# Performance work log

Measured on AMD Instinct MI355X. Metric: run time of the kernel, lower is better.

The kernel has to match this reference:

```python
import jax, jax.numpy as jnp
import numpy as np

N = 100000        # nodes
E = 3200000       # directed edges (already includes both directions per the repo)
F_IN = 256
HID = 16
C = 40


def setup_inputs() -> dict:
    key = jax.random.key(0)
    k = jax.random.split(key, 5)
    x = jax.random.normal(k[0], (N, F_IN), dtype=jnp.float32)
    edge_index = jax.random.randint(k[1], (2, E), 0, N, dtype=jnp.int64)
    W1 = jax.random.normal(k[2], (F_IN, HID), dtype=jnp.float32) * (1.0 / np.sqrt(F_IN))
    b1 = jnp.zeros((HID,), jnp.float32)
    W2 = jax.random.normal(k[3], (HID, C), dtype=jnp.float32) * (1.0 / np.sqrt(HID))
    b2 = jnp.zeros((C,), jnp.float32)
    return {"x": x, "edge_index": edge_index, "W1": W1, "b1": b1, "W2": W2, "b2": b2}


def reference(x, edge_index, W1, b1, W2, b2):
    n = x.shape[0]
    # GCNConv: add self-loops, symmetric degree normalization (shared by both layers)
    loop = jnp.arange(n, dtype=edge_index.dtype)
    src = jnp.concatenate([edge_index[0], loop])
    dst = jnp.concatenate([edge_index[1], loop])
    deg = jax.ops.segment_sum(jnp.ones_like(dst, x.dtype), dst, num_segments=n)
    dinv = jnp.where(deg > 0, jax.lax.rsqrt(deg), 0.0)
    norm = dinv[src] * dinv[dst]  # [E+N]

    def gcn(h, W, b):
        h = h @ W  # transform first (PyG order), keeps edge messages low-dim
        msg = h[src] * norm[:, None]
        return jax.ops.segment_sum(msg, dst, num_segments=n) + b

    h = jax.nn.relu(gcn(x, W1, b1))
    # dropout is identity in eval mode (training=False)
    logits = gcn(h, W2, b2)
    return jax.nn.log_softmax(logits, axis=1)
```

## Files before the change

### kernel.cpp

```cpp
#include <hip/hip_runtime.h>
#include <hip/hip_bf16.h>


#define BSH 7
#define NPB 128
#define BCAP 4736
#define MAXB 1024
#define OVF_CAP 8192
#define EPB 4096

#define SCALE 2097152.0f
#define INVS  4.76837158203125e-7f

typedef __attribute__((ext_vector_type(8))) short bf16x8;
typedef __attribute__((ext_vector_type(4))) short bf16x4;
typedef __attribute__((ext_vector_type(4))) float f32x4;

__device__ __forceinline__ short f2b(float f) {
    __hip_bfloat16 h = __float2bfloat16(f);
    return *reinterpret_cast<short*>(&h);
}
__device__ __forceinline__ float b2f(short s) {
    return __uint_as_float(((unsigned int)(unsigned short)s) << 16);
}

__global__ __launch_bounds__(512) void binA(
        const int* __restrict__ src, const int* __restrict__ dst,
        int* __restrict__ gcur, int* __restrict__ padded,
        int2* __restrict__ ovf, int* __restrict__ ovf_cnt, int E) {
    __shared__ int hist[MAXB], gb[MAXB];
    int tid = threadIdx.x;
    int e0 = blockIdx.x * EPB;
    int e1 = min(e0 + EPB, E);
    for (int b = tid; b < MAXB; b += 512) hist[b] = 0;
    __syncthreads();
    int rs[8], rd[8];
#pragma unroll
    for (int u = 0; u < 8; ++u) {
        int i = e0 + tid + u * 512;
        if (i < e1) {
            rd[u] = dst[i];
            rs[u] = src[i];
            atomicAdd(&hist[rd[u] >> BSH], 1);
        }
    }
    __syncthreads();
    for (int b = tid; b < MAXB; b += 512) {
        int h = hist[b];
        gb[b] = h ? atomicAdd(&gcur[b], h) : 0;
        hist[b] = 0;
    }
    __syncthreads();
#pragma unroll
    for (int u = 0; u < 8; ++u) {
        int i = e0 + tid + u * 512;
        if (i < e1) {
            int s = rs[u], d = rd[u];
            int b = d >> BSH;
            int r = atomicAdd(&hist[b], 1);
            int off = gb[b] + r;
            if (off < BCAP) {
                padded[b * BCAP + off] = (s << BSH) | (d & (NPB - 1));
            } else {
                int k = atomicAdd(ovf_cnt, 1);
                if (k < OVF_CAP) ovf[k] = make_int2(s, d);
            }
        }
    }
}

__global__ __launch_bounds__(512) void gemm1_mfma(
        const float* __restrict__ x, const float* __restrict__ W1,
        const int* __restrict__ gcur, const int* __restrict__ padded,
        float* __restrict__ dinv, short* __restrict__ t1b, int n) {
    __shared__ __align__(16) short xs[128 * 264];
    __shared__ short w1s[256 * 16];
    __shared__ int bins[NPB];
    int tid = threadIdx.x;
    int k = blockIdx.x;
    int base = k * 128;
    int rows = n - base; if (rows > 128) rows = 128;

    if (tid < NPB) bins[tid] = 0;
    for (int i = tid; i < 4096; i += 512) w1s[i] = f2b(W1[i]);
    __syncthreads();

    int ebase = k * BCAP;
    int ecnt = min(gcur[k], BCAP);
    for (int i = tid; i < ecnt; i += 512)
        atomicAdd(&bins[padded[ebase + i] & (NPB - 1)], 1);

    for (int i = tid; i < 8192; i += 512) {
        int r = i >> 6, c = i & 63;
        if (r < rows) {
            float4 v = ((const float4*)(x + (size_t)(base + r) * 256))[c];
            short4 b;
            b.x = f2b(v.x); b.y = f2b(v.y); b.z = f2b(v.z); b.w = f2b(v.w);
            *(short4*)&xs[r * 264 + c * 4] = b;
        }
    }
    __syncthreads();

    int lane = tid & 63, wave = tid >> 6;
    int q = lane >> 4, m = lane & 15;

    bf16x8 bfrag[8];
#pragma unroll
    for (int t = 0; t < 8; ++t)
#pragma unroll
        for (int j = 0; j < 8; ++j)
            bfrag[t][j] = w1s[(t * 32 + q * 8 + j) * 16 + m];

    f32x4 acc = {0.f, 0.f, 0.f, 0.f};
    int arow = wave * 16 + m;
#pragma unroll
    for (int t = 0; t < 8; ++t) {
        bf16x8 a = *(const bf16x8*)&xs[arow * 264 + t * 32 + q * 8];
        acc = __builtin_amdgcn_mfma_f32_16x16x32_bf16(a, bfrag[t], acc, 0, 0, 0);
    }
#pragma unroll
    for (int r = 0; r < 4; ++r) {
        int nl = wave * 16 + q * 4 + r;
        int node = base + nl;
        if (node < n) {
            float di = rsqrtf((float)bins[nl] + 1.0f);
            t1b[(size_t)node * 16 + m] = f2b(acc[r] * di);
            if (m == 0) dinv[node] = di;
        }
    }
}

template <int PHASE>
__global__ __launch_bounds__(512) void aggI(
        const int* __restrict__ gcur, const int* __restrict__ padded,
        const short* __restrict__ feat,
        short* __restrict__ Hout, const float* __restrict__ dinv,
        const float* __restrict__ b1,
        const float* __restrict__ W2, const float* __restrict__ b2,
        float* __restrict__ out, int n) {
    __shared__ int acc[NPB][17];
    __shared__ float W2s[640];
    __shared__ float b2s[40];
    int tid = threadIdx.x, k = blockIdx.x;
    if (PHASE == 1) {
        for (int i = tid; i < 640; i += 512) W2s[i] = W2[i];
        if (tid < 40) b2s[tid] = b2[tid];
    }
    for (int i = tid; i < NPB * 17; i += 512) ((int*)acc)[i] = 0;
    __syncthreads();

    int base = k * BCAP;
    int cnt = min(gcur[k], BCAP);
    const bf16x4* f4 = (const bf16x4*)feat;
    int q = tid & 3, slot = tid >> 2;
    int i = slot;
    for (; i + 896 < cnt; i += 1024) {
        int v0 = padded[base + i];
        int v1 = padded[base + i + 128];
        int v2 = padded[base + i + 256];
        int v3 = padded[base + i + 384];
        int v4 = padded[base + i + 512];
        int v5 = padded[base + i + 640];
        int v6 = padded[base + i + 768];
        int v7 = padded[base + i + 896];
        bf16x4 g0 = f4[(size_t)(v0 >> BSH) * 4 + q];
        bf16x4 g1 = f4[(size_t)(v1 >> BSH) * 4 + q];
        bf16x4 g2 = f4[(size_t)(v2 >> BSH) * 4 + q];
        bf16x4 g3 = f4[(size_t)(v3 >> BSH) * 4 + q];
        bf16x4 g4 = f4[(size_t)(v4 >> BSH) * 4 + q];
        bf16x4 g5 = f4[(size_t)(v5 >> BSH) * 4 + q];
        bf16x4 g6 = f4[(size_t)(v6 >> BSH) * 4 + q];
        bf16x4 g7 = f4[(size_t)(v7 >> BSH) * 4 + q];
        int d0 = v0 & (NPB - 1), d1 = v1 & (NPB - 1);
        int d2 = v2 & (NPB - 1), d3 = v3 & (NPB - 1);
        int d4 = v4 & (NPB - 1), d5 = v5 & (NPB - 1);
        int d6 = v6 & (NPB - 1), d7 = v7 & (NPB - 1);
#pragma unroll
        for (int h = 0; h < 4; ++h) {
            atomicAdd(&acc[d0][q * 4 + h], __float2int_rn(b2f(g0[h]) * SCALE));
            atomicAdd(&acc[d1][q * 4 + h], __float2int_rn(b2f(g1[h]) * SCALE));
            atomicAdd(&acc[d2][q * 4 + h], __float2int_rn(b2f(g2[h]) * SCALE));
            atomicAdd(&acc[d3][q * 4 + h], __float2int_rn(b2f(g3[h]) * SCALE));
            atomicAdd(&acc[d4][q * 4 + h], __float2int_rn(b2f(g4[h]) * SCALE));
            atomicAdd(&acc[d5][q * 4 + h], __float2int_rn(b2f(g5[h]) * SCALE));
            atomicAdd(&acc[d6][q * 4 + h], __float2int_rn(b2f(g6[h]) * SCALE));
            atomicAdd(&acc[d7][q * 4 + h], __float2int_rn(b2f(g7[h]) * SCALE));
        }
    }
    for (; i < cnt; i += 128) {
        int v = padded[base + i];
        bf16x4 g = f4[(size_t)(v >> BSH) * 4 + q];
        int dl = v & (NPB - 1);
#pragma unroll
        for (int h = 0; h < 4; ++h)
            atomicAdd(&acc[dl][q * 4 + h], __float2int_rn(b2f(g[h]) * SCALE));
    }
    __syncthreads();

    int nl = tid >> 2;
    int node = (k << BSH) + nl;
    bool live = node < n;
    if (PHASE == 0) {
        if (live) {
            float di = dinv[node];
            bf16x4 sv = f4[(size_t)node * 4 + q];
            float4 bb = ((const float4*)b1)[q];
            float s0 = b2f(sv[0]) + acc[nl][q * 4 + 0] * INVS;
            float s1 = b2f(sv[1]) + acc[nl][q * 4 + 1] * INVS;
            float s2 = b2f(sv[2]) + acc[nl][q * 4 + 2] * INVS;
            float s3 = b2f(sv[3]) + acc[nl][q * 4 + 3] * INVS;
            bf16x4 o4_;
            o4_[0] = f2b(fmaxf(bb.x + di * s0, 0.f) * di);
            o4_[1] = f2b(fmaxf(bb.y + di * s1, 0.f) * di);
            o4_[2] = f2b(fmaxf(bb.z + di * s2, 0.f) * di);
            o4_[3] = f2b(fmaxf(bb.w + di * s3, 0.f) * di);
            ((bf16x4*)Hout)[(size_t)node * 4 + q] = o4_;
        }
    } else {
        float di = live ? dinv[node] : 0.f;
        float g[16];
        if (live) {
            bf16x8 s0 = ((const bf16x8*)feat)[(size_t)node * 2];
            bf16x8 s1 = ((const bf16x8*)feat)[(size_t)node * 2 + 1];
#pragma unroll
            for (int h = 0; h < 8; ++h) {
                g[h]     = di * (b2f(s0[h]) + acc[nl][h] * INVS);
                g[h + 8] = di * (b2f(s1[h]) + acc[nl][h + 8] * INVS);
            }
        } else {
#pragma unroll
            for (int h = 0; h < 16; ++h) g[h] = 0.f;
        }
        float lg[10];
        float mx = -1e30f;
#pragma unroll
        for (int jj = 0; jj < 10; ++jj) {
            int col = q * 10 + jj;
            float a = b2s[col];
#pragma unroll
            for (int kk = 0; kk < 16; ++kk) a += g[kk] * W2s[kk * 40 + col];
            lg[jj] = a;
            mx = fmaxf(mx, a);
        }
        mx = fmaxf(mx, __shfl_xor(mx, 1));
        mx = fmaxf(mx, __shfl_xor(mx, 2));
        float sum = 0.f;
#pragma unroll
        for (int jj = 0; jj < 10; ++jj) sum += __expf(lg[jj] - mx);
        sum += __shfl_xor(sum, 1);
        sum += __shfl_xor(sum, 2);
        float lse = mx + logf(sum);
        if (live) {
            float2* o2 = (float2*)(out + (size_t)node * 40 + q * 10);
#pragma unroll
            for (int jj = 0; jj < 5; ++jj)
                o2[jj] = make_float2(lg[2 * jj] - lse, lg[2 * jj + 1] - lse);
        }
    }
}

extern "C" void kernel_launch(void* const* d_in, const int* in_sizes, int n_in,
                              void* d_out, int out_size, void* d_ws, size_t ws_size,
                              hipStream_t stream) {
    const float* x  = (const float*)d_in[0];
    const int*   ei = (const int*)d_in[1];
    const float* W1 = (const float*)d_in[2];
    const float* b1 = (const float*)d_in[3];
    const float* W2 = (const float*)d_in[4];
    const float* b2 = (const float*)d_in[5];

    int n = in_sizes[0] / 256;
    int E = in_sizes[1] / 2;
    const int* srcp = ei;
    const int* dstp = ei + E;

    int nbuckets = (n + NPB - 1) >> BSH;

    int*   gcur    = (int*)d_ws;
    int*   ovf_cnt = gcur + MAXB;
    float* dinv    = (float*)(ovf_cnt + 16);
    int2*  ovf     = (int2*)(dinv + n);
    short* t1b     = (short*)(ovf + OVF_CAP);
    short* hdb     = t1b + 16 * (size_t)n;
    int*   padded  = (int*)(hdb + 16 * (size_t)n);
    float* out     = (float*)d_out;

    hipMemsetAsync(gcur, 0, (size_t)(MAXB + 16) * sizeof(int), stream);
    binA      <<<(E + EPB - 1) / EPB, 512, 0, stream>>>(srcp, dstp, gcur, padded,
                                                        ovf, ovf_cnt, E);
    gemm1_mfma<<<nbuckets, 512, 0, stream>>>(x, W1, gcur, padded, dinv, t1b, n);
    aggI<0>   <<<nbuckets, 512, 0, stream>>>(gcur, padded, t1b, hdb, dinv,
                                             b1, nullptr, nullptr, nullptr, n);
    aggI<1>   <<<nbuckets, 512, 0, stream>>>(gcur, padded, hdb, nullptr, dinv,
                                             nullptr, W2, b2, out, n);
}
```

Measured before the change: 285.8 us.

## Run edge binning and layer-1 GEMM concurrently in one role-split kernel

Merges the edge-binning kernel and the x·W1 MFMA GEMM into a single launch whose blocks alternate between the two roles, so the bandwidth-heavy read of x overlaps with the atomic-heavy binning. Because the GEMM no longer waits on binning, it writes unscaled fp32 results. A new small kernel then counts per-node degrees, applies dinv scaling and converts to bf16. This adds an extra fp32 intermediate written and read back, plus one more kernel launch.

```diff
diff --git a/kernel.cpp b/kernel.cpp
--- a/kernel.cpp
+++ b/kernel.cpp
@@ -24,109 +24,125 @@
     return __uint_as_float(((unsigned int)(unsigned short)s) << 16);
 }
 
-__global__ __launch_bounds__(512) void binA(
+__global__ __launch_bounds__(512) void binA_gemm1(
         const int* __restrict__ src, const int* __restrict__ dst,
         int* __restrict__ gcur, int* __restrict__ padded,
-        int2* __restrict__ ovf, int* __restrict__ ovf_cnt, int E) {
-    __shared__ int hist[MAXB], gb[MAXB];
-    int tid = threadIdx.x;
-    int e0 = blockIdx.x * EPB;
-    int e1 = min(e0 + EPB, E);
-    for (int b = tid; b < MAXB; b += 512) hist[b] = 0;
-    __syncthreads();
-    int rs[8], rd[8];
-#pragma unroll
-    for (int u = 0; u < 8; ++u) {
-        int i = e0 + tid + u * 512;
-        if (i < e1) {
-            rd[u] = dst[i];
-            rs[u] = src[i];
-            atomicAdd(&hist[rd[u] >> BSH], 1);
-        }
-    }
-    __syncthreads();
-    for (int b = tid; b < MAXB; b += 512) {
-        int h = hist[b];
-        gb[b] = h ? atomicAdd(&gcur[b], h) : 0;
-        hist[b] = 0;
-    }
-    __syncthreads();
-#pragma unroll
-    for (int u = 0; u < 8; ++u) {
-        int i = e0 + tid + u * 512;
-        if (i < e1) {
-            int s = rs[u], d = rd[u];
-            int b = d >> BSH;
-            int r = atomicAdd(&hist[b], 1);
-            int off = gb[b] + r;
-            if (off < BCAP) {
-                padded[b * BCAP + off] = (s << BSH) | (d & (NPB - 1));
-            } else {
-                int k = atomicAdd(ovf_cnt, 1);
-                if (k < OVF_CAP) ovf[k] = make_int2(s, d);
-            }
-        }
-    }
-}
-
-__global__ __launch_bounds__(512) void gemm1_mfma(
+        int2* __restrict__ ovf, int* __restrict__ ovf_cnt, int E,
         const float* __restrict__ x, const float* __restrict__ W1,
-        const int* __restrict__ gcur, const int* __restrict__ padded,
-        float* __restrict__ dinv, short* __restrict__ t1b, int n) {
+        float* __restrict__ t1raw, int n, int nbA, int nbG) {
     __shared__ __align__(16) short xs[128 * 264];
     __shared__ short w1s[256 * 16];
+    int tid = threadIdx.x;
+    int role = blockIdx.x & 1;
+    int idx  = blockIdx.x >> 1;
+
+    if (role == 0) {
+        if (idx >= nbA) return;
+        int* hist = (int*)xs;
+        int* gb   = hist + MAXB;
+        int e0 = idx * EPB;
+        int e1 = min(e0 + EPB, E);
+        for (int b = tid; b < MAXB; b += 512) hist[b] = 0;
+        __syncthreads();
+        int rs[8], rd[8];
+#pragma unroll
+        for (int u = 0; u < 8; ++u) {
+            int i = e0 + tid + u * 512;
+            if (i < e1) {
+                rd[u] = dst[i];
+                rs[u] = src[i];
+                atomicAdd(&hist[rd[u] >> BSH], 1);
+            }
+        }
+        __syncthreads();
+        for (int b = tid; b < MAXB; b += 512) {
+            int h = hist[b];
+            gb[b] = h ? atomicAdd(&gcur[b], h) : 0;
+            hist[b] = 0;
+        }
+        __syncthreads();
+#pragma unroll
+        for (int u = 0; u < 8; ++u) {
+            int i = e0 + tid + u * 512;
+            if (i < e1) {
+                int s = rs[u], d = rd[u];
+                int b = d >> BSH;
+                int r = atomicAdd(&hist[b], 1);
+                int off = gb[b] + r;
+                if (off < BCAP) {
+                    padded[b * BCAP + off] = (s << BSH) | (d & (NPB - 1));
+                } else {
+                    int k = atomicAdd(ovf_cnt, 1);
+                    if (k < OVF_CAP) ovf[k] = make_int2(s, d);
+                }
+            }
+        }
+    } else {
+        if (idx >= nbG) return;
+        int base = idx * 128;
+        int rows = n - base; if (rows > 128) rows = 128;
+
+        for (int i = tid; i < 4096; i += 512) w1s[i] = f2b(W1[i]);
+        for (int i = tid; i < 8192; i += 512) {
+            int r = i >> 6, c = i & 63;
+            if (r < rows) {
+                float4 v = ((const float4*)(x + (size_t)(base + r) * 256))[c];
+                short4 b;
+                b.x = f2b(v.x); b.y = f2b(v.y); b.z = f2b(v.z); b.w = f2b(v.w);
+                *(short4*)&xs[r * 264 + c * 4] = b;
+            }
+        }
+        __syncthreads();
+
+        int lane = tid & 63, wave = tid >> 6;
+        int q = lane >> 4, m = lane & 15;
+
+        bf16x8 bfrag[8];
+#pragma unroll
+        for (int t = 0; t < 8; ++t)
+#pragma unroll
+            for (int j = 0; j < 8; ++j)
+                bfrag[t][j] = w1s[(t * 32 + q * 8 + j) * 16 + m];
+
+        f32x4 acc = {0.f, 0.f, 0.f, 0.f};
+        int arow = wave * 16 + m;
+#pragma unroll
+        for (int t = 0; t < 8; ++t) {
+            bf16x8 a = *(const bf16x8*)&xs[arow * 264 + t * 32 + q * 8];
+            acc = __builtin_amdgcn_mfma_f32_16x16x32_bf16(a, bfrag[t], acc, 0, 0, 0);
+        }
+#pragma unroll
+        for (int r = 0; r < 4; ++r) {
+            int node = base + wave * 16 + q * 4 + r;
+            if (node < n)
+                t1raw[(size_t)node * 16 + m] = acc[r];
+        }
+    }
+}
+
+__global__ __launch_bounds__(512) void scaledinv(
+        const int* __restrict__ gcur, const int* __restrict__ padded,
+        const float* __restrict__ t1raw, short* __restrict__ t1b,
+        float* __restrict__ dinv, int n) {
     __shared__ int bins[NPB];
-    int tid = threadIdx.x;
-    int k = blockIdx.x;
-    int base = k * 128;
-    int rows = n - base; if (rows > 128) rows = 128;
-
+    int k = blockIdx.x, tid = threadIdx.x;
     if (tid < NPB) bins[tid] = 0;
-    for (int i = tid; i < 4096; i += 512) w1s[i] = f2b(W1[i]);
     __syncthreads();
-
-    int ebase = k * BCAP;
-    int ecnt = min(gcur[k], BCAP);
-    for (int i = tid; i < ecnt; i += 512)
-        atomicAdd(&bins[padded[ebase + i] & (NPB - 1)], 1);
-
-    for (int i = tid; i < 8192; i += 512) {
-        int r = i >> 6, c = i & 63;
-        if (r < rows) {
-            float4 v = ((const float4*)(x + (size_t)(base + r) * 256))[c];
-            short4 b;
-            b.x = f2b(v.x); b.y = f2b(v.y); b.z = f2b(v.z); b.w = f2b(v.w);
-            *(short4*)&xs[r * 264 + c * 4] = b;
-        }
-    }
+    int base = k * BCAP;
+    int cnt = min(gcur[k], BCAP);
+    for (int i = tid; i < cnt; i += 512)
+        atomicAdd(&bins[padded[base + i] & (NPB - 1)], 1);
     __syncthreads();
-
-    int lane = tid & 63, wave = tid >> 6;
-    int q = lane >> 4, m = lane & 15;
-
-    bf16x8 bfrag[8];
-#pragma unroll
-    for (int t = 0; t < 8; ++t)
-#pragma unroll
-        for (int j = 0; j < 8; ++j)
-            bfrag[t][j] = w1s[(t * 32 + q * 8 + j) * 16 + m];
-
-    f32x4 acc = {0.f, 0.f, 0.f, 0.f};
-    int arow = wave * 16 + m;
-#pragma unroll
-    for (int t = 0; t < 8; ++t) {
-        bf16x8 a = *(const bf16x8*)&xs[arow * 264 + t * 32 + q * 8];
-        acc = __builtin_amdgcn_mfma_f32_16x16x32_bf16(a, bfrag[t], acc, 0, 0, 0);
-    }
-#pragma unroll
-    for (int r = 0; r < 4; ++r) {
-        int nl = wave * 16 + q * 4 + r;
-        int node = base + nl;
-        if (node < n) {
-            float di = rsqrtf((float)bins[nl] + 1.0f);
-            t1b[(size_t)node * 16 + m] = f2b(acc[r] * di);
-            if (m == 0) dinv[node] = di;
-        }
+    int nl = tid >> 2, q = tid & 3;
+    int node = (k << BSH) + nl;
+    if (node < n) {
+        float di = rsqrtf((float)bins[nl] + 1.0f);
+        float4 v = ((const float4*)(t1raw + (size_t)node * 16))[q];
+        bf16x4 o;
+        o[0] = f2b(v.x * di); o[1] = f2b(v.y * di);
+        o[2] = f2b(v.z * di); o[3] = f2b(v.w * di);
+        ((bf16x4*)t1b)[(size_t)node * 4 + q] = o;
+        if (q == 0) dinv[node] = di;
     }
 }
 
@@ -275,20 +291,25 @@
     const int* dstp = ei + E;
 
     int nbuckets = (n + NPB - 1) >> BSH;
+    int nbA = (E + EPB - 1) / EPB;
 
     int*   gcur    = (int*)d_ws;
     int*   ovf_cnt = gcur + MAXB;
     float* dinv    = (float*)(ovf_cnt + 16);
     int2*  ovf     = (int2*)(dinv + n);
-    short* t1b     = (short*)(ovf + OVF_CAP);
+    float* t1raw   = (float*)(ovf + OVF_CAP);
+    short* t1b     = (short*)(t1raw + 16 * (size_t)n);
     short* hdb     = t1b + 16 * (size_t)n;
     int*   padded  = (int*)(hdb + 16 * (size_t)n);
     float* out     = (float*)d_out;
 
+    int nb = (nbA > nbuckets) ? nbA : nbuckets;
+
     hipMemsetAsync(gcur, 0, (size_t)(MAXB + 16) * sizeof(int), stream);
-    binA      <<<(E + EPB - 1) / EPB, 512, 0, stream>>>(srcp, dstp, gcur, padded,
-                                                        ovf, ovf_cnt, E);
-    gemm1_mfma<<<nbuckets, 512, 0, stream>>>(x, W1, gcur, padded, dinv, t1b, n);
+    binA_gemm1<<<2 * nb, 512, 0, stream>>>(srcp, dstp, gcur, padded, ovf,
+                                           ovf_cnt, E, x, W1, t1raw, n,
+                                           nbA, nbuckets);
+    scaledinv <<<nbuckets, 512, 0, stream>>>(gcur, padded, t1raw, t1b, dinv, n);
     aggI<0>   <<<nbuckets, 512, 0, stream>>>(gcur, padded, t1b, hdb, dinv,
                                              b1, nullptr, nullptr, nullptr, n);
     aggI<1>   <<<nbuckets, 512, 0, stream>>>(gcur, padded, hdb, nullptr, dinv,
```

Result: faster. 270.6 us (-5.3%).
